# Optimization experiments

Measured on AMD Instinct MI355X. Metric: run time of the kernel, lower is better.

## Reference

```python
import jax, jax.numpy as jnp
import numpy as np

# ---- config (from init_kwargs) ----
PRE_NMS_THRESH = 0.05
K = 200                    # pre_nms_top_n (fixed-size top-k for jit)
NUM_CLASSES = 80
FPN_STRIDE = 8
MASK_SCALE_FACTOR = 2
MASK_STRIDE = FPN_STRIDE / MASK_SCALE_FACTOR  # 4.0
IMG_H, IMG_W = 768, 768


def setup_inputs() -> dict:
    key = jax.random.key(0)
    ks = jax.random.split(key, 6)
    N, C, H, W, DIM = 2, NUM_CLASSES, 96, 96, 32
    # FCOS-style locations for the stride-8 level: center of each cell
    ys, xs = jnp.meshgrid(jnp.arange(H, dtype=jnp.float32),
                          jnp.arange(W, dtype=jnp.float32), indexing='ij')
    locations = jnp.stack([xs.reshape(-1), ys.reshape(-1)], axis=1) * FPN_STRIDE + FPN_STRIDE // 2
    return {
        'locations': locations,                                                 # [HW, 2]
        'box_cls': jax.random.normal(ks[0], (N, C, H, W), jnp.float32) - 2.0,   # mostly below thresh
        'box_regression': jax.random.uniform(ks[1], (N, 4, H, W), jnp.float32) * 100.0,
        'centerness': jax.random.normal(ks[2], (N, 1, H, W), jnp.float32),
        'proposal_embed': jax.random.normal(ks[3], (N, DIM, H, W), jnp.float32),
        'proposal_margin': jax.random.uniform(ks[4], (N, 1, H, W), jnp.float32, minval=0.1, maxval=2.0),
        'pixel_embed': jax.random.normal(ks[5], (N, DIM, 192, 192), jnp.float32),
    }


def reference(locations, box_cls, box_regression, centerness,
              proposal_embed, proposal_margin, pixel_embed):
    N, C, H, W = box_cls.shape
    DIM = proposal_embed.shape[1]
    o_h = pixel_embed.shape[2] * MASK_SCALE_FACTOR
    o_w = pixel_embed.shape[3] * MASK_SCALE_FACTOR

    # interpolate(pixel_embed, size=(o_h, o_w), mode='bilinear', align_corners=False)
    pix_up = jax.image.resize(pixel_embed, (N, DIM, o_h, o_w), method='bilinear')

    # NCHW -> [N, HW, C] flattening (matches permute(0,2,3,1).reshape)
    scores = jax.nn.sigmoid(jnp.transpose(box_cls.reshape(N, C, H * W), (0, 2, 1)))   # [N, HW, C]
    ctr = jax.nn.sigmoid(centerness.reshape(N, H * W))                                # [N, HW]
    reg = jnp.transpose(box_regression.reshape(N, 4, H * W), (0, 2, 1))               # [N, HW, 4]
    emb = jnp.transpose(proposal_embed.reshape(N, DIM, H * W), (0, 2, 1))             # [N, HW, DIM]
    mar = proposal_margin.reshape(N, H * W)                                           # [N, HW]

    xs = jnp.arange(o_w, dtype=jnp.float32)
    ys = jnp.arange(o_h, dtype=jnp.float32)

    def per_image(s, c, r, e, m, pix):
        # threshold + centerness-weighted score; invalid candidates rank last
        cand = s > PRE_NMS_THRESH                       # [HW, C]
        sc = s * c[:, None]                             # [HW, C]
        flat = jnp.where(cand, sc, -1.0).reshape(-1)    # [HW*C]
        topv, topi = jax.lax.top_k(flat, K)             # fixed-size top-k
        loc_idx = topi // C                             # [K]
        labels = topi % C + 1                           # [K]
        valid = topv > 0.0                              # padded slots when < K candidates

        # box decode: [x - l, y - t, x + r, y + b], clipped to image
        loc = locations[loc_idx]                        # [K, 2]
        rr = r[loc_idx]                                 # [K, 4]
        x1 = jnp.clip(loc[:, 0] - rr[:, 0], 0.0, IMG_W - 1)
        y1 = jnp.clip(loc[:, 1] - rr[:, 1], 0.0, IMG_H - 1)
        x2 = jnp.clip(loc[:, 0] + rr[:, 2], 0.0, IMG_W - 1)
        y2 = jnp.clip(loc[:, 1] + rr[:, 3], 0.0, IMG_H - 1)
        boxes = jnp.stack([x1, y1, x2, y2], axis=1)     # [K, 4]

        # boxes_to_masks at mask stride: binary inside-box masks [K, o_h, o_w]
        mb = boxes / MASK_STRIDE
        in_x = (xs[None, :] >= mb[:, 0:1]) & (xs[None, :] <= mb[:, 2:3])  # [K, o_w]
        in_y = (ys[None, :] >= mb[:, 1:2]) & (ys[None, :] <= mb[:, 3:4])  # [K, o_h]
        box_mask = in_y[:, :, None] & in_x[:, None, :]

        # pixel-embed distance mask: exp(-||pix - e_k||^2 * margin_k)
        ek = e[loc_idx]                                 # [K, DIM]
        mk = m[loc_idx]                                 # [K]
        p = pix.reshape(DIM, o_h * o_w)                 # [DIM, P]
        d2 = (jnp.sum(ek * ek, axis=1)[:, None]
              + jnp.sum(p * p, axis=0)[None, :]
              - 2.0 * ek @ p)                           # [K, P] via GEMM
        prob = jnp.exp(-d2 * mk[:, None]).reshape(K, o_h, o_w)
        masks = prob * box_mask.astype(prob.dtype) * valid[:, None, None].astype(prob.dtype)
        return masks

    masks = jax.vmap(per_image)(scores, ctr, reg, emb, mar, pix_up)  # [N, K, o_h, o_w]
    return masks
```

## Files before the change

kernel.cpp:

```cpp
#include <hip/hip_runtime.h>
#include <cmath>


namespace {
constexpr int NIMG = 2;
constexpr int NC   = 80;
constexpr int NHW  = 96 * 96;
constexpr int NCHW = NC * NHW;
constexpr int NDIM = 32;
constexpr int PH = 192, PW = 192;
constexpr int OH = 384, OW = 384;
constexpr int KTOP = 200;
constexpr int CAP = 4096;
constexpr int MCAP = 1024;
constexpr int LCAP = 512;
constexpr float PRE_THRESH = 0.05f;
constexpr unsigned KEY_ZERO = 0x80000000u;
constexpr float IMG_MAX = 767.0f;

constexpr int NBOX = NIMG * KTOP;
constexpr int ZTILES = 6;
constexpr int NZB = NBOX * ZTILES;

constexpr int NF4 = NCHW / 4;
constexpr int SEL_BLOCKS = 128;
constexpr int NSEL = 2 * SEL_BLOCKS;
constexpr int SEL_STRIDE = SEL_BLOCKS * 256;
constexpr int SEL_ITERS = (NF4 + SEL_STRIDE - 1) / SEL_STRIDE;

constexpr int WS_HIST1  = 0;
constexpr int WS_CNT    = WS_HIST1 + NIMG * 2048;
constexpr int WS_BAR    = WS_CNT + NIMG;
constexpr int WS_TICK   = WS_BAR + 1;
constexpr int WS_ZERO_WORDS = WS_TICK + NIMG;
constexpr int WS_PAIRS  = 4104;
constexpr int WS_PARAMS = WS_PAIRS + NIMG * CAP * 2;
constexpr int PARAM_WORDS = 40;

typedef float f4 __attribute__((ext_vector_type(4)));
}

__device__ __forceinline__ unsigned key_of(float f) {
  unsigned u = __float_as_uint(f);
  return (u & 0x80000000u) ? ~u : (u | 0x80000000u);
}

__global__ __launch_bounds__(256) void k_zero_ws(unsigned* __restrict__ ws) {
  for (int j = threadIdx.x; j < WS_ZERO_WORDS; j += 256) ws[j] = 0u;
}

__global__ __launch_bounds__(256) void k_main(
    const float* __restrict__ box_cls, const float* __restrict__ ctrness,
    const float* __restrict__ locations, const float* __restrict__ box_reg,
    const float* __restrict__ pemb, const float* __restrict__ pmar,
    unsigned* __restrict__ ws, float* __restrict__ out) {
  const int t = threadIdx.x;
  if (blockIdx.x >= NSEL) {
    const int zb = blockIdx.x - NSEL;
    f4* ob4 = reinterpret_cast<f4*>(out) + (size_t)zb * (64 * OW / 4);
    const f4 z = {0.f, 0.f, 0.f, 0.f};
    #pragma unroll
    for (int i = 0; i < 24; ++i) ob4[i * 256 + t] = z;
    return;
  }

  __shared__ unsigned hist[2048];
  __shared__ unsigned sh_sum[256];
  __shared__ int sh_bk[2];
  __shared__ unsigned loc[LCAP][2];
  __shared__ int lcnt;
  __shared__ unsigned gbase;
  __shared__ int sh_last;
  const int n = blockIdx.x >= SEL_BLOCKS;
  const int bi = blockIdx.x - n * SEL_BLOCKS;

  for (int i = t; i < 2048; i += 256) hist[i] = 0;
  __syncthreads();
  const float* cls = box_cls + n * NCHW;
  const float* ctr = ctrness + n * NHW;
  unsigned kk[SEL_ITERS][4];
  #pragma unroll
  for (int s = 0; s < SEL_ITERS; ++s) {
    const int j4 = s * SEL_STRIDE + bi * 256 + t;
    if (j4 < NF4) {
      const int j = j4 * 4;
      const int c = j / NHW;
      const int hw = j - c * NHW;
      const f4 xv = *reinterpret_cast<const f4*>(cls + j);
      const f4 cv = *reinterpret_cast<const f4*>(ctr + hw);
      #pragma unroll
      for (int q = 0; q < 4; ++q) {
        const float sg = 1.0f / (1.0f + expf(-xv[q]));
        float v = -1.0f;
        if (sg > PRE_THRESH) v = sg * (1.0f / (1.0f + expf(-cv[q])));
        const unsigned k = key_of(v);
        kk[s][q] = k;
        if (k > KEY_ZERO) atomicAdd(&hist[k >> 21], 1u);
      }
    } else {
      #pragma unroll
      for (int q = 0; q < 4; ++q) kk[s][q] = 0u;
    }
  }
  __syncthreads();
  {
    unsigned* gh = ws + WS_HIST1 + n * 2048;
    for (int i = t; i < 2048; i += 256) { unsigned v = hist[i]; if (v) atomicAdd(&gh[i], v); }
  }

  __syncthreads();
  if (t == 0) {
    atomicAdd(ws + WS_BAR, 1u);
    while (__hip_atomic_load(ws + WS_BAR, __ATOMIC_RELAXED,
                             __HIP_MEMORY_SCOPE_AGENT) < (unsigned)NSEL) {
      __builtin_amdgcn_s_sleep(2);
    }
  }
  __syncthreads();

  if (t == 0) { sh_bk[0] = -1; sh_bk[1] = KTOP; }
  {
    const unsigned* gh = ws + WS_HIST1 + n * 2048;
    unsigned local = 0;
    for (int j = 0; j < 8; ++j) { unsigned v = gh[t * 8 + j]; hist[t * 8 + j] = v; local += v; }
    sh_sum[t] = local;
  }
  __syncthreads();
  {
    unsigned S = 0;
    for (int j = t + 1; j < 256; ++j) S += sh_sum[j];
    int cand_b = -1;
    unsigned cand_above = 0;
    unsigned run = S;
    for (int j = 7; j >= 0; --j) {
      const unsigned cv = hist[t * 8 + j];
      if (cand_b < 0 && run + cv >= (unsigned)KTOP) { cand_b = t * 8 + j; cand_above = run; }
      run += cv;
    }
    if (cand_b >= 0) atomicMax(&sh_bk[0], cand_b);
    __syncthreads();
    if (cand_b >= 0 && cand_b == sh_bk[0]) sh_bk[1] = KTOP - (int)cand_above;
    __syncthreads();
  }
  const unsigned b1 = (unsigned)(sh_bk[0] < 0 ? 0 : sh_bk[0]);
  int krem = sh_bk[1];

  if (t == 0) lcnt = 0;
  __syncthreads();
  #pragma unroll
  for (int s = 0; s < SEL_ITERS; ++s) {
    #pragma unroll
    for (int q = 0; q < 4; ++q) {
      const unsigned k = kk[s][q];
      if ((k >> 21) < b1) continue;
      const int j = (s * SEL_STRIDE + bi * 256 + t) * 4 + q;
      const int c = j / NHW;
      const int hw = j - c * NHW;
      const int p = atomicAdd(&lcnt, 1);
      if (p < LCAP) { loc[p][0] = k; loc[p][1] = (unsigned)(hw * NC + c); }
    }
  }
  __syncthreads();
  const int lc = min(lcnt, LCAP);
  if (t == 0) gbase = atomicAdd(ws + WS_CNT + n, (unsigned)lc);
  __syncthreads();
  for (int i = t; i < lc; i += 256) {
    const unsigned pos = gbase + (unsigned)i;
    if (pos < (unsigned)CAP) {
      __hip_atomic_store(&ws[WS_PAIRS + (n * CAP + (int)pos) * 2], loc[i][0],
                         __ATOMIC_RELAXED, __HIP_MEMORY_SCOPE_AGENT);
      __hip_atomic_store(&ws[WS_PAIRS + (n * CAP + (int)pos) * 2 + 1], loc[i][1],
                         __ATOMIC_RELAXED, __HIP_MEMORY_SCOPE_AGENT);
    }
  }

  __syncthreads();
  if (t == 0) {
    const unsigned old = atomicAdd(ws + WS_TICK + n, 1u);
    sh_last = (old == (unsigned)(SEL_BLOCKS - 1)) ? 1 : 0;
  }
  __syncthreads();
  if (!sh_last) return;

  __shared__ uint2 P[CAP];
  __shared__ unsigned h256[256];
  __shared__ unsigned mKey[MCAP], mRef[MCAP];
  __shared__ int sh_b, sh_t;
  for (int s = t; s < KTOP; s += 256) ws[WS_PARAMS + (n * KTOP + s) * PARAM_WORDS] = 0u;
  const int cnt = min((int)__hip_atomic_load(ws + WS_CNT + n, __ATOMIC_RELAXED,
                                             __HIP_MEMORY_SCOPE_AGENT), CAP);
  for (int i = t; i < cnt; i += 256) {
    P[i].x = __hip_atomic_load(&ws[WS_PAIRS + (n * CAP + i) * 2],
                               __ATOMIC_RELAXED, __HIP_MEMORY_SCOPE_AGENT);
    P[i].y = __hip_atomic_load(&ws[WS_PAIRS + (n * CAP + i) * 2 + 1],
                               __ATOMIC_RELAXED, __HIP_MEMORY_SCOPE_AGENT);
  }
  __syncthreads();

  unsigned prefix = b1;
  int shift = 21;
  #pragma unroll
  for (int level = 0; level < 2; ++level) {
    const int newshift = shift - 8;
    h256[t] = 0;
    if (t == 0) sh_b = 0;
    __syncthreads();
    for (int i = t; i < cnt; i += 256) {
      const unsigned k = P[i].x;
      if ((k >> shift) == prefix) atomicAdd(&h256[(k >> newshift) & 255u], 1u);
    }
    __syncthreads();
    const unsigned hv = h256[t];
    unsigned S = 0;
    for (int j = t + 1; j < 256; ++j) S += h256[j];
    if (S + hv >= (unsigned)krem) atomicMax(&sh_b, t);
    __syncthreads();
    const int b = sh_b;
    if (t == b) sh_t = krem - (int)S;
    __syncthreads();
    krem = sh_t;
    prefix = (prefix << 8) | (unsigned)b;
    shift = newshift;
    __syncthreads();
  }

  if (t == 0) sh_t = 0;
  __syncthreads();
  for (int i = t; i < cnt; i += 256) {
    const unsigned k = P[i].x;
    if ((k >> 5) >= prefix) {
      const int pos = atomicAdd(&sh_t, 1);
      if (pos < MCAP) { mKey[pos] = k; mRef[pos] = P[i].y; }
    }
  }
  __syncthreads();
  const int m = min(sh_t, MCAP);

  for (int i = t; i < m; i += 256) {
    const unsigned ki = mKey[i], ri = mRef[i];
    int rank = 0;
    for (int j = 0; j < m; ++j) {
      const unsigned kj = mKey[j], rj = mRef[j];
      rank += (kj > ki || (kj == ki && rj < ri)) ? 1 : 0;
    }
    if (rank >= KTOP) continue;
    unsigned* pp = ws + WS_PARAMS + (n * KTOP + rank) * PARAM_WORDS;
    int valid = 0;
    if (ki > KEY_ZERO) {
      const int hw = (int)ri / NC;
      const float lx = locations[2 * hw], ly = locations[2 * hw + 1];
      const float rl = box_reg[(n * 4 + 0) * NHW + hw];
      const float rt = box_reg[(n * 4 + 1) * NHW + hw];
      const float rr = box_reg[(n * 4 + 2) * NHW + hw];
      const float rb = box_reg[(n * 4 + 3) * NHW + hw];
      const float x1 = fminf(fmaxf(lx - rl, 0.f), IMG_MAX);
      const float y1 = fminf(fmaxf(ly - rt, 0.f), IMG_MAX);
      const float x2 = fminf(fmaxf(lx + rr, 0.f), IMG_MAX);
      const float y2 = fminf(fmaxf(ly + rb, 0.f), IMG_MAX);
      const int ix0 = max(0, (int)ceilf(x1 * 0.25f));
      const int ix1 = min(OW - 1, (int)floorf(x2 * 0.25f));
      const int iy0 = max(0, (int)ceilf(y1 * 0.25f));
      const int iy1 = min(OH - 1, (int)floorf(y2 * 0.25f));
      if (ix0 <= ix1 && iy0 <= iy1) {
        valid = 1;
        pp[1] = (unsigned)ix0; pp[2] = (unsigned)ix1;
        pp[3] = (unsigned)iy0; pp[4] = (unsigned)iy1;
        reinterpret_cast<float*>(pp)[5] = pmar[n * NHW + hw];
        float* ep = reinterpret_cast<float*>(pp) + 8;
        #pragma unroll
        for (int d = 0; d < NDIM; ++d) ep[d] = pemb[(n * NDIM + d) * NHW + hw];
      }
    }
    pp[0] = (unsigned)valid;
  }
}

__global__ __launch_bounds__(256) void k_box(const float* __restrict__ pix,
                                             const unsigned* __restrict__ ws,
                                             float* __restrict__ out) {
  const int nk = blockIdx.x;
  const int t = threadIdx.x;
  const unsigned* meta = ws + WS_PARAMS + nk * PARAM_WORDS;
  if (meta[0] == 0u) return;
  const int ix0 = (int)meta[1], ix1 = (int)meta[2];
  const int iy0 = (int)meta[3], iy1 = (int)meta[4];
  const float margin = __uint_as_float(meta[5]);
  float e[NDIM];
  {
    const float4* e4 = reinterpret_cast<const float4*>(meta + 8);
    #pragma unroll
    for (int q = 0; q < NDIM / 4; ++q) {
      const float4 v = e4[q];
      e[4 * q + 0] = v.x; e[4 * q + 1] = v.y; e[4 * q + 2] = v.z; e[4 * q + 3] = v.w;
    }
  }
  const int n = nk / KTOP;
  const float* peb = pix + (size_t)n * NDIM * PH * PW;
  float* ob = out + (size_t)nk * (OH * OW);

  const int tx = t & 63;
  const int ts = t >> 6;
  const int h = iy1 - iy0 + 1;
  const int shh = (h + 3) >> 2;
  const int ybeg = iy0 + ts * shh;
  const int yend = min(iy0 + (ts + 1) * shh, iy1 + 1);

  for (int c = ix0 + tx; c <= ix1; c += 64) {
    const float sx = 0.5f * (float)c - 0.25f;
    const float xf = floorf(sx);
    const float fx = sx - xf;
    const int xs0 = max((int)xf, 0);
    const int xs1 = min((int)xf + 1, PW - 1);
    float qa_[NDIM], qb_[NDIM];
    int ra = -9, rb = -9;
    for (int y = ybeg; y < yend; ++y) {
      const float sy = 0.5f * (float)y - 0.25f;
      const float yf = floorf(sy);
      const float fy = sy - yf;
      const int ys0 = max((int)yf, 0);
      const int ys1 = min((int)yf + 1, PH - 1);
      if (ys0 != ra) {
        if (ys0 == rb) {
          #pragma unroll
          for (int d = 0; d < NDIM; ++d) qa_[d] = qb_[d];
        } else {
          const float* p = peb + (size_t)ys0 * PW;
          #pragma unroll
          for (int d = 0; d < NDIM; ++d)
            qa_[d] = (1.f - fx) * p[d * PH * PW + xs0] + fx * p[d * PH * PW + xs1];
        }
        ra = ys0;
      }
      if (ys1 != rb) {
        if (ys1 == ra) {
          #pragma unroll
          for (int d = 0; d < NDIM; ++d) qb_[d] = qa_[d];
        } else {
          const float* p = peb + (size_t)ys1 * PW;
          #pragma unroll
          for (int d = 0; d < NDIM; ++d)
            qb_[d] = (1.f - fx) * p[d * PH * PW + xs0] + fx * p[d * PH * PW + xs1];
        }
        rb = ys1;
      }
      float d2 = 0.f;
      #pragma unroll
      for (int d = 0; d < NDIM; ++d) {
        const float pv = qa_[d] + fy * (qb_[d] - qa_[d]);
        const float df = e[d] - pv;
        d2 = fmaf(df, df, d2);
      }
      ob[(size_t)y * OW + c] = expf(-d2 * margin);
    }
  }
}

extern "C" void kernel_launch(void* const* d_in, const int* in_sizes, int n_in,
                              void* d_out, int out_size, void* d_ws, size_t ws_size,
                              hipStream_t stream) {
  const float* locations = (const float*)d_in[0];
  const float* box_cls   = (const float*)d_in[1];
  const float* box_reg   = (const float*)d_in[2];
  const float* ctrness   = (const float*)d_in[3];
  const float* pemb      = (const float*)d_in[4];
  const float* pmar      = (const float*)d_in[5];
  const float* pix       = (const float*)d_in[6];
  float* out = (float*)d_out;
  unsigned* ws = (unsigned*)d_ws;

  k_zero_ws<<<dim3(1), dim3(256), 0, stream>>>(ws);
  k_main  <<<dim3(NSEL + NZB), dim3(256), 0, stream>>>(
      box_cls, ctrness, locations, box_reg, pemb, pmar, ws, out);
  k_box   <<<dim3(NBOX), dim3(256), 0, stream>>>(pix, ws, out);
}
```

Before: 104.9 us.

## Fuse box-mask kernel into persistent main kernel with grid barrier and tile pool

```diff
diff --git a/kernel.cpp b/kernel.cpp
--- a/kernel.cpp
+++ b/kernel.cpp
@@ -20,20 +20,24 @@
 
 constexpr int NBOX = NIMG * KTOP;
 constexpr int ZTILES = 6;
-constexpr int NZB = NBOX * ZTILES;
+constexpr int NTILES = NBOX * ZTILES;
+constexpr int TILE_F4 = 64 * OW / 4;
 
 constexpr int NF4 = NCHW / 4;
 constexpr int SEL_BLOCKS = 128;
 constexpr int NSEL = 2 * SEL_BLOCKS;
+constexpr int GRID = 512;
 constexpr int SEL_STRIDE = SEL_BLOCKS * 256;
 constexpr int SEL_ITERS = (NF4 + SEL_STRIDE - 1) / SEL_STRIDE;
 
-constexpr int WS_HIST1  = 0;
-constexpr int WS_CNT    = WS_HIST1 + NIMG * 2048;
-constexpr int WS_BAR    = WS_CNT + NIMG;
-constexpr int WS_TICK   = WS_BAR + 1;
-constexpr int WS_ZERO_WORDS = WS_TICK + NIMG;
-constexpr int WS_PAIRS  = 4104;
+constexpr int WS_HIST1 = 0;
+constexpr int WS_CNT   = WS_HIST1 + NIMG * 2048;
+constexpr int WS_BAR1  = WS_CNT + NIMG;
+constexpr int WS_BAR2  = WS_BAR1 + 1;
+constexpr int WS_TICK  = WS_BAR2 + 1;
+constexpr int WS_POOL  = WS_TICK + NIMG;
+constexpr int WS_ZERO_WORDS = WS_POOL + 1;
+constexpr int WS_PAIRS = 4104;
 constexpr int WS_PARAMS = WS_PAIRS + NIMG * CAP * 2;
 constexpr int PARAM_WORDS = 40;
 
@@ -44,258 +48,262 @@
   unsigned u = __float_as_uint(f);
   return (u & 0x80000000u) ? ~u : (u | 0x80000000u);
 }
+__device__ __forceinline__ unsigned aget(const unsigned* p) {
+  return __hip_atomic_load(p, __ATOMIC_RELAXED, __HIP_MEMORY_SCOPE_AGENT);
+}
+__device__ __forceinline__ void aput(unsigned* p, unsigned v) {
+  __hip_atomic_store(p, v, __ATOMIC_RELAXED, __HIP_MEMORY_SCOPE_AGENT);
+}
 
 __global__ __launch_bounds__(256) void k_zero_ws(unsigned* __restrict__ ws) {
   for (int j = threadIdx.x; j < WS_ZERO_WORDS; j += 256) ws[j] = 0u;
 }
 
-__global__ __launch_bounds__(256) void k_main(
+__global__ __launch_bounds__(256, 2) void k_main(
     const float* __restrict__ box_cls, const float* __restrict__ ctrness,
     const float* __restrict__ locations, const float* __restrict__ box_reg,
     const float* __restrict__ pemb, const float* __restrict__ pmar,
+    const float* __restrict__ pix,
     unsigned* __restrict__ ws, float* __restrict__ out) {
   const int t = threadIdx.x;
-  if (blockIdx.x >= NSEL) {
-    const int zb = blockIdx.x - NSEL;
-    f4* ob4 = reinterpret_cast<f4*>(out) + (size_t)zb * (64 * OW / 4);
-    const f4 z = {0.f, 0.f, 0.f, 0.f};
-    #pragma unroll
-    for (int i = 0; i < 24; ++i) ob4[i * 256 + t] = z;
-    return;
-  }
-
+  const int bid = blockIdx.x;
   __shared__ unsigned hist[2048];
   __shared__ unsigned sh_sum[256];
   __shared__ int sh_bk[2];
   __shared__ unsigned loc[LCAP][2];
-  __shared__ int lcnt;
+  __shared__ unsigned mKey[MCAP], mRef[MCAP];
+  __shared__ unsigned h256[256];
+  __shared__ int lcnt, sh_last, sh_b, sh_t2, sh_tk;
   __shared__ unsigned gbase;
-  __shared__ int sh_last;
-  const int n = blockIdx.x >= SEL_BLOCKS;
-  const int bi = blockIdx.x - n * SEL_BLOCKS;
-
-  for (int i = t; i < 2048; i += 256) hist[i] = 0;
-  __syncthreads();
-  const float* cls = box_cls + n * NCHW;
-  const float* ctr = ctrness + n * NHW;
-  unsigned kk[SEL_ITERS][4];
-  #pragma unroll
-  for (int s = 0; s < SEL_ITERS; ++s) {
-    const int j4 = s * SEL_STRIDE + bi * 256 + t;
-    if (j4 < NF4) {
-      const int j = j4 * 4;
-      const int c = j / NHW;
-      const int hw = j - c * NHW;
-      const f4 xv = *reinterpret_cast<const f4*>(cls + j);
-      const f4 cv = *reinterpret_cast<const f4*>(ctr + hw);
+
+  if (bid < NSEL) {
+    const int n = bid >= SEL_BLOCKS;
+    const int bi = bid - n * SEL_BLOCKS;
+
+    for (int i = t; i < 2048; i += 256) hist[i] = 0;
+    __syncthreads();
+    const float* cls = box_cls + n * NCHW;
+    const float* ctr = ctrness + n * NHW;
+    unsigned kk[SEL_ITERS][4];
+    #pragma unroll
+    for (int s = 0; s < SEL_ITERS; ++s) {
+      const int j4 = s * SEL_STRIDE + bi * 256 + t;
+      if (j4 < NF4) {
+        const int j = j4 * 4;
+        const int c = j / NHW;
+        const int hw = j - c * NHW;
+        const f4 xv = *reinterpret_cast<const f4*>(cls + j);
+        const f4 cv = *reinterpret_cast<const f4*>(ctr + hw);
+        #pragma unroll
+        for (int q = 0; q < 4; ++q) {
+          const float sg = 1.0f / (1.0f + expf(-xv[q]));
+          float v = -1.0f;
+          if (sg > PRE_THRESH) v = sg * (1.0f / (1.0f + expf(-cv[q])));
+          const unsigned k = key_of(v);
+          kk[s][q] = k;
+          if (k > KEY_ZERO) atomicAdd(&hist[k >> 21], 1u);
+        }
+      } else {
+        #pragma unroll
+        for (int q = 0; q < 4; ++q) kk[s][q] = 0u;
+      }
+    }
+    __syncthreads();
+    {
+      unsigned* gh = ws + WS_HIST1 + n * 2048;
+      for (int i = t; i < 2048; i += 256) { unsigned v = hist[i]; if (v) atomicAdd(&gh[i], v); }
+    }
+
+    __syncthreads();
+    if (t == 0) {
+      __hip_atomic_fetch_add(ws + WS_BAR1, 1u, __ATOMIC_ACQ_REL, __HIP_MEMORY_SCOPE_AGENT);
+      while (__hip_atomic_load(ws + WS_BAR1, __ATOMIC_ACQUIRE,
+                               __HIP_MEMORY_SCOPE_AGENT) < (unsigned)NSEL) {
+        __builtin_amdgcn_s_sleep(8);
+      }
+    }
+    __syncthreads();
+
+    if (t == 0) { sh_bk[0] = -1; sh_bk[1] = KTOP; }
+    {
+      const unsigned* gh = ws + WS_HIST1 + n * 2048;
+      unsigned local = 0;
+      for (int j = 0; j < 8; ++j) { unsigned v = gh[t * 8 + j]; hist[t * 8 + j] = v; local += v; }
+      sh_sum[t] = local;
+    }
+    __syncthreads();
+    {
+      unsigned S = 0;
+      for (int j = t + 1; j < 256; ++j) S += sh_sum[j];
+      int cand_b = -1;
+      unsigned cand_above = 0;
+      unsigned run = S;
+      for (int j = 7; j >= 0; --j) {
+        const unsigned cv = hist[t * 8 + j];
+        if (cand_b < 0 && run + cv >= (unsigned)KTOP) { cand_b = t * 8 + j; cand_above = run; }
+        run += cv;
+      }
+      if (cand_b >= 0) atomicMax(&sh_bk[0], cand_b);
+      __syncthreads();
+      if (cand_b >= 0 && cand_b == sh_bk[0]) sh_bk[1] = KTOP - (int)cand_above;
+      __syncthreads();
+    }
+    const unsigned b1 = (unsigned)(sh_bk[0] < 0 ? 0 : sh_bk[0]);
+    int krem = sh_bk[1];
+
+    if (t == 0) lcnt = 0;
+    __syncthreads();
+    #pragma unroll
+    for (int s = 0; s < SEL_ITERS; ++s) {
       #pragma unroll
       for (int q = 0; q < 4; ++q) {
-        const float sg = 1.0f / (1.0f + expf(-xv[q]));
-        float v = -1.0f;
-        if (sg > PRE_THRESH) v = sg * (1.0f / (1.0f + expf(-cv[q])));
-        const unsigned k = key_of(v);
-        kk[s][q] = k;
-        if (k > KEY_ZERO) atomicAdd(&hist[k >> 21], 1u);
-      }
-    } else {
+        const unsigned k = kk[s][q];
+        if ((k >> 21) < b1) continue;
+        const int j = (s * SEL_STRIDE + bi * 256 + t) * 4 + q;
+        const int c = j / NHW;
+        const int hw = j - c * NHW;
+        const int p = atomicAdd(&lcnt, 1);
+        if (p < LCAP) { loc[p][0] = k; loc[p][1] = (unsigned)(hw * NC + c); }
+      }
+    }
+    __syncthreads();
+    const int lc = min(lcnt, LCAP);
+    if (t == 0) gbase = atomicAdd(ws + WS_CNT + n, (unsigned)lc);
+    __syncthreads();
+    for (int i = t; i < lc; i += 256) {
+      const unsigned pos = gbase + (unsigned)i;
+      if (pos < (unsigned)CAP) {
+        aput(&ws[WS_PAIRS + (n * CAP + (int)pos) * 2], loc[i][0]);
+        aput(&ws[WS_PAIRS + (n * CAP + (int)pos) * 2 + 1], loc[i][1]);
+      }
+    }
+
+    __syncthreads();
+    if (t == 0) {
+      const unsigned old = atomicAdd(ws + WS_TICK + n, 1u);
+      sh_last = (old == (unsigned)(SEL_BLOCKS - 1)) ? 1 : 0;
+    }
+    __syncthreads();
+
+    if (sh_last) {
+      for (int s = t; s < KTOP; s += 256) aput(&ws[WS_PARAMS + (n * KTOP + s) * PARAM_WORDS], 0u);
+      const int cnt = min((int)aget(ws + WS_CNT + n), CAP);
+      unsigned prefix = b1;
+      int shift = 21;
       #pragma unroll
-      for (int q = 0; q < 4; ++q) kk[s][q] = 0u;
+      for (int level = 0; level < 2; ++level) {
+        const int newshift = shift - 8;
+        h256[t] = 0;
+        if (t == 0) sh_b = 0;
+        __syncthreads();
+        for (int i = t; i < cnt; i += 256) {
+          const unsigned k = aget(&ws[WS_PAIRS + (n * CAP + i) * 2]);
+          if ((k >> shift) == prefix) atomicAdd(&h256[(k >> newshift) & 255u], 1u);
+        }
+        __syncthreads();
+        const unsigned hv = h256[t];
+        unsigned S = 0;
+        for (int j = t + 1; j < 256; ++j) S += h256[j];
+        if (S + hv >= (unsigned)krem) atomicMax(&sh_b, t);
+        __syncthreads();
+        const int b = sh_b;
+        if (t == b) sh_t2 = krem - (int)S;
+        __syncthreads();
+        krem = sh_t2;
+        prefix = (prefix << 8) | (unsigned)b;
+        shift = newshift;
+        __syncthreads();
+      }
+
+      if (t == 0) sh_t2 = 0;
+      __syncthreads();
+      for (int i = t; i < cnt; i += 256) {
+        const unsigned k = aget(&ws[WS_PAIRS + (n * CAP + i) * 2]);
+        if ((k >> 5) >= prefix) {
+          const int pos = atomicAdd(&sh_t2, 1);
+          if (pos < MCAP) { mKey[pos] = k; mRef[pos] = aget(&ws[WS_PAIRS + (n * CAP + i) * 2 + 1]); }
+        }
+      }
+      __syncthreads();
+      const int m = min(sh_t2, MCAP);
+
+      for (int i = t; i < m; i += 256) {
+        const unsigned ki = mKey[i], ri = mRef[i];
+        int rank = 0;
+        for (int j = 0; j < m; ++j) {
+          const unsigned kj = mKey[j], rj = mRef[j];
+          rank += (kj > ki || (kj == ki && rj < ri)) ? 1 : 0;
+        }
+        if (rank >= KTOP) continue;
+        unsigned* pp = ws + WS_PARAMS + (n * KTOP + rank) * PARAM_WORDS;
+        int valid = 0;
+        if (ki > KEY_ZERO) {
+          const int hw = (int)ri / NC;
+          const float lx = locations[2 * hw], ly = locations[2 * hw + 1];
+          const float rl = box_reg[(n * 4 + 0) * NHW + hw];
+          const float rt = box_reg[(n * 4 + 1) * NHW + hw];
+          const float rr = box_reg[(n * 4 + 2) * NHW + hw];
+          const float rb = box_reg[(n * 4 + 3) * NHW + hw];
+          const float x1 = fminf(fmaxf(lx - rl, 0.f), IMG_MAX);
+          const float y1 = fminf(fmaxf(ly - rt, 0.f), IMG_MAX);
+          const float x2 = fminf(fmaxf(lx + rr, 0.f), IMG_MAX);
+          const float y2 = fminf(fmaxf(ly + rb, 0.f), IMG_MAX);
+          const int ix0 = max(0, (int)ceilf(x1 * 0.25f));
+          const int ix1 = min(OW - 1, (int)floorf(x2 * 0.25f));
+          const int iy0 = max(0, (int)ceilf(y1 * 0.25f));
+          const int iy1 = min(OH - 1, (int)floorf(y2 * 0.25f));
+          if (ix0 <= ix1 && iy0 <= iy1) {
+            valid = 1;
+            aput(pp + 1, (unsigned)ix0); aput(pp + 2, (unsigned)ix1);
+            aput(pp + 3, (unsigned)iy0); aput(pp + 4, (unsigned)iy1);
+            aput(pp + 5, __float_as_uint(pmar[n * NHW + hw]));
+            #pragma unroll
+            for (int d = 0; d < NDIM; ++d)
+              aput(pp + 8 + d, __float_as_uint(pemb[(n * NDIM + d) * NHW + hw]));
+          }
+        }
+        aput(pp + 0, (unsigned)valid);
+      }
+      __syncthreads();
+    }
+  }
+
+  {
+    const f4 z = {0.f, 0.f, 0.f, 0.f};
+    for (;;) {
+      if (t == 0) sh_tk = (int)atomicAdd(ws + WS_POOL, 1u);
+      __syncthreads();
+      const int tk = sh_tk;
+      __syncthreads();
+      if (tk >= NTILES) break;
+      f4* ob4 = reinterpret_cast<f4*>(out) + (size_t)tk * TILE_F4;
+      #pragma unroll
+      for (int i = 0; i < 24; ++i) ob4[i * 256 + t] = z;
+    }
+  }
+
+  __syncthreads();
+  if (t == 0) {
+    __hip_atomic_fetch_add(ws + WS_BAR2, 1u, __ATOMIC_ACQ_REL, __HIP_MEMORY_SCOPE_AGENT);
+    while (__hip_atomic_load(ws + WS_BAR2, __ATOMIC_ACQUIRE,
+                             __HIP_MEMORY_SCOPE_AGENT) < (unsigned)GRID) {
+      __builtin_amdgcn_s_sleep(8);
     }
   }
   __syncthreads();
-  {
-    unsigned* gh = ws + WS_HIST1 + n * 2048;
-    for (int i = t; i < 2048; i += 256) { unsigned v = hist[i]; if (v) atomicAdd(&gh[i], v); }
-  }
-
-  __syncthreads();
-  if (t == 0) {
-    atomicAdd(ws + WS_BAR, 1u);
-    while (__hip_atomic_load(ws + WS_BAR, __ATOMIC_RELAXED,
-                             __HIP_MEMORY_SCOPE_AGENT) < (unsigned)NSEL) {
-      __builtin_amdgcn_s_sleep(2);
-    }
-  }
-  __syncthreads();
-
-  if (t == 0) { sh_bk[0] = -1; sh_bk[1] = KTOP; }
-  {
-    const unsigned* gh = ws + WS_HIST1 + n * 2048;
-    unsigned local = 0;
-    for (int j = 0; j < 8; ++j) { unsigned v = gh[t * 8 + j]; hist[t * 8 + j] = v; local += v; }
-    sh_sum[t] = local;
-  }
-  __syncthreads();
-  {
-    unsigned S = 0;
-    for (int j = t + 1; j < 256; ++j) S += sh_sum[j];
-    int cand_b = -1;
-    unsigned cand_above = 0;
-    unsigned run = S;
-    for (int j = 7; j >= 0; --j) {
-      const unsigned cv = hist[t * 8 + j];
-      if (cand_b < 0 && run + cv >= (unsigned)KTOP) { cand_b = t * 8 + j; cand_above = run; }
-      run += cv;
-    }
-    if (cand_b >= 0) atomicMax(&sh_bk[0], cand_b);
-    __syncthreads();
-    if (cand_b >= 0 && cand_b == sh_bk[0]) sh_bk[1] = KTOP - (int)cand_above;
-    __syncthreads();
-  }
-  const unsigned b1 = (unsigned)(sh_bk[0] < 0 ? 0 : sh_bk[0]);
-  int krem = sh_bk[1];
-
-  if (t == 0) lcnt = 0;
-  __syncthreads();
+
+  if (bid >= NBOX) return;
+  const int nk = bid;
+  const unsigned* meta = ws + WS_PARAMS + nk * PARAM_WORDS;
+  if (aget(meta) == 0u) return;
+  const int ix0 = (int)aget(meta + 1), ix1 = (int)aget(meta + 2);
+  const int iy0 = (int)aget(meta + 3), iy1 = (int)aget(meta + 4);
+  const float margin = __uint_as_float(aget(meta + 5));
+  float e[NDIM];
   #pragma unroll
-  for (int s = 0; s < SEL_ITERS; ++s) {
-    #pragma unroll
-    for (int q = 0; q < 4; ++q) {
-      const unsigned k = kk[s][q];
-      if ((k >> 21) < b1) continue;
-      const int j = (s * SEL_STRIDE + bi * 256 + t) * 4 + q;
-      const int c = j / NHW;
-      const int hw = j - c * NHW;
-      const int p = atomicAdd(&lcnt, 1);
-      if (p < LCAP) { loc[p][0] = k; loc[p][1] = (unsigned)(hw * NC + c); }
-    }
-  }
-  __syncthreads();
-  const int lc = min(lcnt, LCAP);
-  if (t == 0) gbase = atomicAdd(ws + WS_CNT + n, (unsigned)lc);
-  __syncthreads();
-  for (int i = t; i < lc; i += 256) {
-    const unsigned pos = gbase + (unsigned)i;
-    if (pos < (unsigned)CAP) {
-      __hip_atomic_store(&ws[WS_PAIRS + (n * CAP + (int)pos) * 2], loc[i][0],
-                         __ATOMIC_RELAXED, __HIP_MEMORY_SCOPE_AGENT);
-      __hip_atomic_store(&ws[WS_PAIRS + (n * CAP + (int)pos) * 2 + 1], loc[i][1],
-                         __ATOMIC_RELAXED, __HIP_MEMORY_SCOPE_AGENT);
-    }
-  }
-
-  __syncthreads();
-  if (t == 0) {
-    const unsigned old = atomicAdd(ws + WS_TICK + n, 1u);
-    sh_last = (old == (unsigned)(SEL_BLOCKS - 1)) ? 1 : 0;
-  }
-  __syncthreads();
-  if (!sh_last) return;
-
-  __shared__ uint2 P[CAP];
-  __shared__ unsigned h256[256];
-  __shared__ unsigned mKey[MCAP], mRef[MCAP];
-  __shared__ int sh_b, sh_t;
-  for (int s = t; s < KTOP; s += 256) ws[WS_PARAMS + (n * KTOP + s) * PARAM_WORDS] = 0u;
-  const int cnt = min((int)__hip_atomic_load(ws + WS_CNT + n, __ATOMIC_RELAXED,
-                                             __HIP_MEMORY_SCOPE_AGENT), CAP);
-  for (int i = t; i < cnt; i += 256) {
-    P[i].x = __hip_atomic_load(&ws[WS_PAIRS + (n * CAP + i) * 2],
-                               __ATOMIC_RELAXED, __HIP_MEMORY_SCOPE_AGENT);
-    P[i].y = __hip_atomic_load(&ws[WS_PAIRS + (n * CAP + i) * 2 + 1],
-                               __ATOMIC_RELAXED, __HIP_MEMORY_SCOPE_AGENT);
-  }
-  __syncthreads();
-
-  unsigned prefix = b1;
-  int shift = 21;
-  #pragma unroll
-  for (int level = 0; level < 2; ++level) {
-    const int newshift = shift - 8;
-    h256[t] = 0;
-    if (t == 0) sh_b = 0;
-    __syncthreads();
-    for (int i = t; i < cnt; i += 256) {
-      const unsigned k = P[i].x;
-      if ((k >> shift) == prefix) atomicAdd(&h256[(k >> newshift) & 255u], 1u);
-    }
-    __syncthreads();
-    const unsigned hv = h256[t];
-    unsigned S = 0;
-    for (int j = t + 1; j < 256; ++j) S += h256[j];
-    if (S + hv >= (unsigned)krem) atomicMax(&sh_b, t);
-    __syncthreads();
-    const int b = sh_b;
-    if (t == b) sh_t = krem - (int)S;
-    __syncthreads();
-    krem = sh_t;
-    prefix = (prefix << 8) | (unsigned)b;
-    shift = newshift;
-    __syncthreads();
-  }
-
-  if (t == 0) sh_t = 0;
-  __syncthreads();
-  for (int i = t; i < cnt; i += 256) {
-    const unsigned k = P[i].x;
-    if ((k >> 5) >= prefix) {
-      const int pos = atomicAdd(&sh_t, 1);
-      if (pos < MCAP) { mKey[pos] = k; mRef[pos] = P[i].y; }
-    }
-  }
-  __syncthreads();
-  const int m = min(sh_t, MCAP);
-
-  for (int i = t; i < m; i += 256) {
-    const unsigned ki = mKey[i], ri = mRef[i];
-    int rank = 0;
-    for (int j = 0; j < m; ++j) {
-      const unsigned kj = mKey[j], rj = mRef[j];
-      rank += (kj > ki || (kj == ki && rj < ri)) ? 1 : 0;
-    }
-    if (rank >= KTOP) continue;
-    unsigned* pp = ws + WS_PARAMS + (n * KTOP + rank) * PARAM_WORDS;
-    int valid = 0;
-    if (ki > KEY_ZERO) {
-      const int hw = (int)ri / NC;
-      const float lx = locations[2 * hw], ly = locations[2 * hw + 1];
-      const float rl = box_reg[(n * 4 + 0) * NHW + hw];
-      const float rt = box_reg[(n * 4 + 1) * NHW + hw];
-      const float rr = box_reg[(n * 4 + 2) * NHW + hw];
-      const float rb = box_reg[(n * 4 + 3) * NHW + hw];
-      const float x1 = fminf(fmaxf(lx - rl, 0.f), IMG_MAX);
-      const float y1 = fminf(fmaxf(ly - rt, 0.f), IMG_MAX);
-      const float x2 = fminf(fmaxf(lx + rr, 0.f), IMG_MAX);
-      const float y2 = fminf(fmaxf(ly + rb, 0.f), IMG_MAX);
-      const int ix0 = max(0, (int)ceilf(x1 * 0.25f));
-      const int ix1 = min(OW - 1, (int)floorf(x2 * 0.25f));
-      const int iy0 = max(0, (int)ceilf(y1 * 0.25f));
-      const int iy1 = min(OH - 1, (int)floorf(y2 * 0.25f));
-      if (ix0 <= ix1 && iy0 <= iy1) {
-        valid = 1;
-        pp[1] = (unsigned)ix0; pp[2] = (unsigned)ix1;
-        pp[3] = (unsigned)iy0; pp[4] = (unsigned)iy1;
-        reinterpret_cast<float*>(pp)[5] = pmar[n * NHW + hw];
-        float* ep = reinterpret_cast<float*>(pp) + 8;
-        #pragma unroll
-        for (int d = 0; d < NDIM; ++d) ep[d] = pemb[(n * NDIM + d) * NHW + hw];
-      }
-    }
-    pp[0] = (unsigned)valid;
-  }
-}
-
-__global__ __launch_bounds__(256) void k_box(const float* __restrict__ pix,
-                                             const unsigned* __restrict__ ws,
-                                             float* __restrict__ out) {
-  const int nk = blockIdx.x;
-  const int t = threadIdx.x;
-  const unsigned* meta = ws + WS_PARAMS + nk * PARAM_WORDS;
-  if (meta[0] == 0u) return;
-  const int ix0 = (int)meta[1], ix1 = (int)meta[2];
-  const int iy0 = (int)meta[3], iy1 = (int)meta[4];
-  const float margin = __uint_as_float(meta[5]);
-  float e[NDIM];
-  {
-    const float4* e4 = reinterpret_cast<const float4*>(meta + 8);
-    #pragma unroll
-    for (int q = 0; q < NDIM / 4; ++q) {
-      const float4 v = e4[q];
-      e[4 * q + 0] = v.x; e[4 * q + 1] = v.y; e[4 * q + 2] = v.z; e[4 * q + 3] = v.w;
-    }
-  }
-  const int n = nk / KTOP;
-  const float* peb = pix + (size_t)n * NDIM * PH * PW;
+  for (int d = 0; d < NDIM; ++d) e[d] = __uint_as_float(aget(meta + 8 + d));
+  const int n2 = nk / KTOP;
+  const float* peb = pix + (size_t)n2 * NDIM * PH * PW;
   float* ob = out + (size_t)nk * (OH * OW);
 
   const int tx = t & 63;
@@ -369,7 +377,6 @@
   unsigned* ws = (unsigned*)d_ws;
 
   k_zero_ws<<<dim3(1), dim3(256), 0, stream>>>(ws);
-  k_main  <<<dim3(NSEL + NZB), dim3(256), 0, stream>>>(
-      box_cls, ctrness, locations, box_reg, pemb, pmar, ws, out);
-  k_box   <<<dim3(NBOX), dim3(256), 0, stream>>>(pix, ws, out);
-}
+  k_main   <<<dim3(GRID), dim3(256), 0, stream>>>(
+      box_cls, ctrness, locations, box_reg, pemb, pmar, pix, ws, out);
+}
```

New measurement: 373.6 us. 3.56x slower.
